# Performance work log

Measured on AMD Instinct MI355X. Metric: run time of the kernel, lower is better.

Reference implementation:

```python
import jax, jax.numpy as jnp
import numpy as np
from math import sqrt


def setup_inputs() -> dict:
    key = jax.random.key(0)
    ks = jax.random.split(key, 10)
    N, C = 192, 96  # C = N // 2
    n, h, w = 8, 64, 64
    s = lambda fan_in: 1.0 / np.sqrt(fan_in)
    return {
        "x": jax.random.normal(ks[0], (n, N, h, w), dtype=jnp.float32),
        "pe": jax.random.normal(ks[1], (N, 120, 120), dtype=jnp.float32) * 0.02,
        "wq": jax.random.normal(ks[2], (C, N), dtype=jnp.float32) * s(N),
        "bq": jax.random.normal(ks[3], (C,), dtype=jnp.float32) * 0.01,
        "wk": jax.random.normal(ks[4], (C, N), dtype=jnp.float32) * s(N),
        "bk": jax.random.normal(ks[5], (C,), dtype=jnp.float32) * 0.01,
        "wv": jax.random.normal(ks[6], (C, N), dtype=jnp.float32) * s(N),
        "bv": jax.random.normal(ks[7], (C,), dtype=jnp.float32) * 0.01,
        "wz": jax.random.normal(ks[8], (N, C), dtype=jnp.float32) * s(C),
        "bz": jax.random.normal(ks[9], (N,), dtype=jnp.float32) * 0.01,
    }


def _conv1x1(x, w, b):
    # x: [n, cin, h, w]; w: [cout, cin]; b: [cout]
    return jnp.einsum("oc,nchw->nohw", w, x) + b[None, :, None, None]


def reference(x, pe, wq, bq, wk, bk, wv, bv, wz, bz):
    n, c_in, h, w = x.shape
    hw = h * w
    # 2D positional encoding, sliced to the actual spatial size
    x = x + pe[None, :, :h, :w]
    c = wq.shape[0]  # N // 2
    q = _conv1x1(x, wq, bq).reshape(n, c, hw)   # [n, c, hw]
    k = _conv1x1(x, wk, bk).reshape(n, c, hw)   # [n, c, hw]
    v = _conv1x1(x, wv, bv).reshape(n, c, hw)   # [n, c, hw]
    scale = sqrt(hw)
    # logits[n, i, j] = sum_c q[n,c,i] * k[n,c,j]
    logits = jnp.einsum("nci,ncj->nij", q, k) / scale  # [n, hw, hw]
    weights = jax.nn.softmax(logits, axis=-1)
    # z[n, c, i] = sum_j weights[n,i,j] * v[n,c,j]
    z = jnp.einsum("nij,ncj->nci", weights, v).reshape(n, c, h, w)
    z = _conv1x1(z, wz, bz)  # [n, N, h, w]
    return x + z
```

## Files before the change

kernel.cpp:

```cpp
#include <hip/hip_runtime.h>
#include <hip/hip_bf16.h>

#define HW 4096
#define CIN 192
#define CMID 96

typedef __attribute__((ext_vector_type(8))) short bf16x8;
typedef __attribute__((ext_vector_type(4))) float f32x4;
typedef __attribute__((ext_vector_type(16))) float f32x16;
typedef __attribute__((ext_vector_type(4))) unsigned int u32x4;
typedef __attribute__((ext_vector_type(2))) unsigned int u32x2;

static __device__ __forceinline__ unsigned short f2bf(float f) {
    union { float f; unsigned int u; } v;
    v.f = f;
    unsigned int r = v.u + 0x7fffu + ((v.u >> 16) & 1u);
    return (unsigned short)(r >> 16);
}

static __device__ __forceinline__ void gload16(const void* g, void* l) {
    __builtin_amdgcn_global_load_lds(
        (const __attribute__((address_space(1))) unsigned int*)g,
        (__attribute__((address_space(3))) unsigned int*)l, 16, 0, 0);
}

#define SCQ (0.015625f * 1.44269504089f)

__global__ __launch_bounds__(256) void convw_kernel(
    const float* __restrict__ wq, const float* __restrict__ wk,
    const float* __restrict__ wv, const float* __restrict__ wz,
    unsigned short* __restrict__ wqkvb, unsigned short* __restrict__ wzb)
{
    int idx = blockIdx.x * 256 + threadIdx.x;
    if (idx < 3 * CMID * CIN) {
        int m = idx / (CMID * CIN), r = idx % (CMID * CIN);
        const float* w = (m == 0) ? wq : ((m == 1) ? wk : wv);
        wqkvb[idx] = f2bf(w[r]);
    } else if (idx < 3 * CMID * CIN + CIN * CMID) {
        int r = idx - 3 * CMID * CIN;
        wzb[r] = f2bf(wz[r]);
    }
}

__global__ __launch_bounds__(512) void qkv_kernel(
    const float* __restrict__ x, const float* __restrict__ pe,
    const unsigned short* __restrict__ wqkvb,
    const float* __restrict__ bq, const float* __restrict__ bk,
    const float* __restrict__ bv,
    unsigned short* __restrict__ Q, unsigned short* __restrict__ K,
    unsigned short* __restrict__ V)
{
    const int n = blockIdx.y, bx = blockIdx.x, i0 = bx * 64, t = threadIdx.x;
    __shared__ unsigned short xt[64 * 200];

    #pragma unroll
    for (int it = 0; it < 6; ++it) {
        int q = t + it * 512;
        int c = q >> 4, il4 = (q & 15) << 2;
        f32x4 xv = *(const f32x4*)(x + ((size_t)n * CIN + c) * HW + i0 + il4);
        f32x4 pv = *(const f32x4*)(pe + c * 14400 + bx * 120 + il4);
        float a0 = xv[0] + pv[0], a1 = xv[1] + pv[1];
        float a2 = xv[2] + pv[2], a3 = xv[3] + pv[3];
        unsigned w01, w23;
        asm("v_cvt_pk_bf16_f32 %0, %1, %2" : "=v"(w01) : "v"(a0), "v"(a1));
        asm("v_cvt_pk_bf16_f32 %0, %1, %2" : "=v"(w23) : "v"(a2), "v"(a3));
        xt[(il4 + 0) * 200 + c] = (unsigned short)w01;
        xt[(il4 + 1) * 200 + c] = (unsigned short)(w01 >> 16);
        xt[(il4 + 2) * 200 + c] = (unsigned short)w23;
        xt[(il4 + 3) * 200 + c] = (unsigned short)(w23 >> 16);
    }
    __syncthreads();

    const int w = t >> 6, lane = t & 63, l15 = lane & 15, lg = lane >> 4;
    const int wg = w >> 2;
    const int p0 = (w & 3) * 16;

    bf16x8 af[6];
    #pragma unroll
    for (int f = 0; f < 6; ++f)
        af[f] = *(const bf16x8*)(xt + (p0 + l15) * 200 + f * 32 + lg * 8);

    #pragma unroll
    for (int cc = 0; cc < 9; ++cc) {
        const int ct = wg * 9 + cc;
        const int m = ct / 6, c6 = ct % 6;
        f32x4 acc = (f32x4){0.f, 0.f, 0.f, 0.f};
        const unsigned short* wrow = wqkvb + (ct * 16 + l15) * CIN + lg * 8;
        #pragma unroll
        for (int f = 0; f < 6; ++f) {
            bf16x8 wf = *(const bf16x8*)(wrow + f * 32);
            if (m < 2)
                acc = __builtin_amdgcn_mfma_f32_16x16x32_bf16(wf, af[f], acc, 0, 0, 0);
            else
                acc = __builtin_amdgcn_mfma_f32_16x16x32_bf16(af[f], wf, acc, 0, 0, 0);
        }
        if (m < 2) {
            f32x4 bv4 = *(const f32x4*)(((m == 0) ? bq : bk) + c6 * 16 + lg * 4);
            ushort4 pk4;
            if (m == 0) {
                pk4.x = f2bf((acc[0] + bv4[0]) * SCQ);
                pk4.y = f2bf((acc[1] + bv4[1]) * SCQ);
                pk4.z = f2bf((acc[2] + bv4[2]) * SCQ);
                pk4.w = f2bf((acc[3] + bv4[3]) * SCQ);
            } else {
                pk4.x = f2bf(acc[0] + bv4[0]);
                pk4.y = f2bf(acc[1] + bv4[1]);
                pk4.z = f2bf(acc[2] + bv4[2]);
                pk4.w = f2bf(acc[3] + bv4[3]);
            }
            unsigned short* dst = ((m == 0) ? Q : K) + (size_t)n * HW * CMID;
            *(ushort4*)(dst + (size_t)(i0 + p0 + l15) * CMID + c6 * 16 + lg * 4) = pk4;
        } else {
            const float bias = bv[c6 * 16 + l15];
            ushort4 pk4;
            pk4.x = f2bf(acc[0] + bias); pk4.y = f2bf(acc[1] + bias);
            pk4.z = f2bf(acc[2] + bias); pk4.w = f2bf(acc[3] + bias);
            *(ushort4*)(V + (size_t)n * CMID * HW + (size_t)(c6 * 16 + l15) * HW
                          + i0 + p0 + lg * 4) = pk4;
        }
    }
}

__global__ __launch_bounds__(256, 2) void attn_kernel(
    const unsigned short* __restrict__ Q, const unsigned short* __restrict__ K,
    const unsigned short* __restrict__ V,
    unsigned short* __restrict__ zp, float* __restrict__ lp)
{
    const int bid = blockIdx.x;
    const int n    = bid & 7;
    const int iblk = (bid >> 3) & 15;
    const int js   = bid >> 7;

    const int t = threadIdx.x, w = t >> 6, lane = t & 63;
    const int l31 = lane & 31, hi = lane >> 5;
    const int ib = iblk * 256 + w * 64;

    __shared__ unsigned short Ks[3][32 * 128];
    __shared__ unsigned short Vs[2][96 * 64];

    const unsigned short* Qb = Q + (size_t)n * HW * CMID;
    const unsigned short* Kb = K + (size_t)n * HW * CMID;
    const unsigned short* Vb = V + (size_t)n * CMID * HW;

    bf16x8 qf[2][6];
    #pragma unroll
    for (int is = 0; is < 2; ++is)
        #pragma unroll
        for (int kc = 0; kc < 6; ++kc)
            qf[is][kc] = *(const bf16x8*)(Qb + (size_t)(ib + is * 32 + l31) * CMID
                                            + kc * 16 + hi * 8);

    int ksoff[2], vsoff[3];
    #pragma unroll
    for (int s = 0; s < 2; ++s) {
        int row = 8 * w + 4 * s + (lane >> 4);
        ksoff[s] = row * CMID + (((lane & 15) ^ (row & 7)) * 8);
    }
    #pragma unroll
    for (int s = 0; s < 3; ++s) {
        int c = 8 * (w * 3 + s) + (lane >> 3);
        vsoff[s] = c * HW + (((lane & 7) ^ (c & 7)) * 8);
    }

    const int j00 = js * 1024;

#define STAGE_K(TILE, KB) do {                                                 \
    _Pragma("unroll") for (int s = 0; s < 2; ++s)                              \
        gload16(Kb + (size_t)(j00 + (TILE) * 32) * CMID + ksoff[s],            \
                &Ks[KB][(w * 2 + s) * 512]);                                   \
} while (0)
#define STAGE_V(WND, VB) do {                                                  \
    _Pragma("unroll") for (int s = 0; s < 3; ++s)                              \
        gload16(Vb + (size_t)(j00 + (WND) * 64) + vsoff[s],                    \
                &Vs[VB][(w * 3 + s) * 512]);                                   \
} while (0)

    f32x16 O[2][3], Lon[2];
    #pragma unroll
    for (int is = 0; is < 2; ++is) {
        #pragma unroll
        for (int cc = 0; cc < 3; ++cc)
            #pragma unroll
            for (int e = 0; e < 16; ++e) O[is][cc][e] = 0.f;
        #pragma unroll
        for (int e = 0; e < 16; ++e) Lon[is][e] = 0.f;
    }

    bf16x8 onef;
    #pragma unroll
    for (int e = 0; e < 8; ++e) onef[e] = (short)0x3F80;

    STAGE_K(0, 0);
    STAGE_K(1, 1);
    STAGE_V(0, 0);
    asm volatile("s_waitcnt vmcnt(0)" ::: "memory");
    __builtin_amdgcn_s_barrier();

#define BODY(KBUF, VBUF, VHALF) do {                                           \
    const unsigned short* Kc = &Ks[KBUF][0];                                   \
    const unsigned short* Vc = &Vs[VBUF][0];                                   \
    f32x16 s0, s1;                                                             \
    _Pragma("unroll") for (int e = 0; e < 16; ++e) { s0[e] = 0.f; s1[e] = 0.f; } \
    __builtin_amdgcn_s_setprio(1);                                             \
    _Pragma("unroll") for (int kc = 0; kc < 6; ++kc) {                         \
        bf16x8 kf = *(const bf16x8*)(Kc + l31 * 128 +                          \
                      (((kc * 2 + hi) ^ (l31 & 7)) << 3));                     \
        s0 = __builtin_amdgcn_mfma_f32_32x32x16_bf16(kf, qf[0][kc], s0, 0, 0, 0); \
        s1 = __builtin_amdgcn_mfma_f32_32x32x16_bf16(kf, qf[1][kc], s1, 0, 0, 0); \
    }                                                                          \
    __builtin_amdgcn_s_setprio(0);                                             \
    unsigned pkk[2][4][2];                                                     \
    _Pragma("unroll") for (int q = 0; q < 4; ++q)                              \
        _Pragma("unroll") for (int rp = 0; rp < 2; ++rp) {                     \
            float lo0 = __builtin_exp2f(s0[q * 4 + 2 * rp]);                   \
            float hh0 = __builtin_exp2f(s0[q * 4 + 2 * rp + 1]);               \
            float lo1 = __builtin_exp2f(s1[q * 4 + 2 * rp]);                   \
            float hh1 = __builtin_exp2f(s1[q * 4 + 2 * rp + 1]);               \
            asm("v_cvt_pk_bf16_f32 %0, %1, %2"                                 \
                : "=v"(pkk[0][q][rp]) : "v"(lo0), "v"(hh0));                   \
            asm("v_cvt_pk_bf16_f32 %0, %1, %2"                                 \
                : "=v"(pkk[1][q][rp]) : "v"(lo1), "v"(hh1));                   \
        }                                                                      \
    u32x4 pfu[2][2];                                                           \
    _Pragma("unroll") for (int is = 0; is < 2; ++is)                           \
        _Pragma("unroll") for (int jc = 0; jc < 2; ++jc) {                     \
            unsigned x0 = pkk[is][2 * jc][0], y0 = pkk[is][2 * jc + 1][0];     \
            unsigned x1 = pkk[is][2 * jc][1], y1 = pkk[is][2 * jc + 1][1];     \
            asm("v_permlane32_swap_b32 %0, %1" : "+v"(y0), "+v"(x0));          \
            asm("v_permlane32_swap_b32 %0, %1" : "+v"(y1), "+v"(x1));          \
            pfu[is][jc][0] = x0; pfu[is][jc][1] = x1;                          \
            pfu[is][jc][2] = y0; pfu[is][jc][3] = y1;                          \
        }                                                                      \
    __builtin_amdgcn_s_setprio(1);                                             \
    _Pragma("unroll") for (int jc = 0; jc < 2; ++jc) {                         \
        bf16x8 pa0 = __builtin_bit_cast(bf16x8, pfu[0][jc]);                   \
        bf16x8 pa1 = __builtin_bit_cast(bf16x8, pfu[1][jc]);                   \
        _Pragma("unroll") for (int cc = 0; cc < 3; ++cc) {                     \
            bf16x8 vf = *(const bf16x8*)(Vc + (cc * 32 + l31) * 64 +           \
                          ((((VHALF) * 4 + jc * 2 + hi) ^ (l31 & 7)) << 3));   \
            O[0][cc] = __builtin_amdgcn_mfma_f32_32x32x16_bf16(pa0, vf, O[0][cc], 0, 0, 0); \
            O[1][cc] = __builtin_amdgcn_mfma_f32_32x32x16_bf16(pa1, vf, O[1][cc], 0, 0, 0); \
        }                                                                      \
        Lon[0] = __builtin_amdgcn_mfma_f32_32x32x16_bf16(pa0, onef, Lon[0], 0, 0, 0); \
        Lon[1] = __builtin_amdgcn_mfma_f32_32x32x16_bf16(pa1, onef, Lon[1], 0, 0, 0); \
    }                                                                          \
    __builtin_amdgcn_s_setprio(0);                                             \
} while (0)

    int kb = 0, kb1 = 1, kb2 = 2;
    for (int tt = 0; tt < 32; tt += 2) {
        {
            const int pfk = (tt + 2 < 32) ? tt + 2 : 31;
            STAGE_K(pfk, kb2);
            const int wn = (tt >> 1) + 1;
            const int pfw = (wn < 16) ? wn : 15;
            STAGE_V(pfw, wn & 1);
            BODY(kb, (tt >> 1) & 1, 0);
            asm volatile("s_waitcnt vmcnt(5)" ::: "memory");
            __builtin_amdgcn_s_barrier();
        }
        {
            const int pfk = (tt + 3 < 32) ? tt + 3 : 31;
            STAGE_K(pfk, kb);
            BODY(kb1, (tt >> 1) & 1, 1);
            asm volatile("s_waitcnt vmcnt(2)" ::: "memory");
            __builtin_amdgcn_s_barrier();
        }
        const int tmp = kb;
        kb = kb2; kb2 = kb1; kb1 = tmp;
    }
#undef BODY
#undef STAGE_K
#undef STAGE_V

    asm volatile("s_waitcnt vmcnt(0)" ::: "memory");

    unsigned short* zb = zp + ((size_t)js * 8 + n) * HW * CMID;
    #pragma unroll
    for (int is = 0; is < 2; ++is)
        #pragma unroll
        for (int cc = 0; cc < 3; ++cc)
            #pragma unroll
            for (int r = 0; r < 16; ++r) {
                int i = ib + is * 32 + (r & 3) + 8 * (r >> 2) + 4 * hi;
                zb[(size_t)i * CMID + cc * 32 + l31] = f2bf(O[is][cc][r]);
            }

    if (l31 == 0) {
        float* lb = lp + ((size_t)js * 8 + n) * HW;
        #pragma unroll
        for (int is = 0; is < 2; ++is)
            #pragma unroll
            for (int r = 0; r < 16; ++r) {
                int i = ib + is * 32 + (r & 3) + 8 * (r >> 2) + 4 * hi;
                lb[i] = Lon[is][r];
            }
    }
}

__global__ __launch_bounds__(256) void zproj_kernel(
    const unsigned short* __restrict__ zp, const float* __restrict__ lp,
    const unsigned short* __restrict__ wzb, const float* __restrict__ bz,
    const float* __restrict__ x, const float* __restrict__ pe,
    float* __restrict__ out)
{
    const int n = blockIdx.y, i0 = blockIdx.x * 64, t = threadIdx.x;
    __shared__ unsigned short zt[64 * 104];
    __shared__ float ll[64];

    if (t < 64) {
        float s = 0.f;
        #pragma unroll
        for (int sl = 0; sl < 4; ++sl)
            s += lp[(size_t)sl * 8 * HW + (size_t)n * HW + i0 + t];
        ll[t] = 1.f / s;
    }
    __syncthreads();

    #pragma unroll
    for (int u = 0; u < 3; ++u) {
        int unit = t + u * 256;
        int i = unit / 12, g = unit % 12;
        size_t gidx = ((size_t)n * HW + i0 + i) * CMID + g * 8;
        float a[8];
        #pragma unroll
        for (int e = 0; e < 8; ++e) a[e] = 0.f;
        #pragma unroll
        for (int sl = 0; sl < 4; ++sl) {
            u32x4 wv = *(const u32x4*)(zp + (size_t)sl * 8 * HW * CMID + gidx);
            #pragma unroll
            for (int k = 0; k < 4; ++k) {
                union { unsigned u; float f; } lo, hi2;
                lo.u = wv[k] << 16;
                hi2.u = wv[k] & 0xffff0000u;
                a[2 * k]     += lo.f;
                a[2 * k + 1] += hi2.f;
            }
        }
        float li = ll[i];
        unsigned ww[4];
        #pragma unroll
        for (int k = 0; k < 4; ++k) {
            float p0 = a[2 * k] * li, p1 = a[2 * k + 1] * li;
            asm("v_cvt_pk_bf16_f32 %0, %1, %2" : "=v"(ww[k]) : "v"(p0), "v"(p1));
        }
        u32x4 wv4 = {ww[0], ww[1], ww[2], ww[3]};
        *(u32x4*)(zt + i * 104 + g * 8) = wv4;
    }
    __syncthreads();

    const int w = t >> 6, lane = t & 63, l15 = lane & 15, lg = lane >> 4;
    const int p0 = w * 16;

    bf16x8 af[3];
    #pragma unroll
    for (int f = 0; f < 3; ++f)
        af[f] = *(const bf16x8*)(zt + (p0 + l15) * 104 + f * 32 + lg * 8);

    #pragma unroll
    for (int ct = 0; ct < 12; ++ct) {
        f32x4 acc = (f32x4){0.f, 0.f, 0.f, 0.f};
        const unsigned short* wrow = wzb + (ct * 16 + l15) * CMID + lg * 8;
        #pragma unroll
        for (int f = 0; f < 3; ++f) {
            bf16x8 wf = *(const bf16x8*)(wrow + f * 32);
            acc = __builtin_amdgcn_mfma_f32_16x16x32_bf16(af[f], wf, acc, 0, 0, 0);
        }
        const int co = ct * 16 + l15;
        const int ibase = i0 + p0 + lg * 4;
        size_t xa = ((size_t)n * CIN + co) * HW + ibase;
        f32x4 xv = *(const f32x4*)(x + xa);
        f32x4 pv = *(const f32x4*)(pe + co * 14400 + blockIdx.x * 120 + p0 + lg * 4);
        const float bias = bz[co];
        f32x4 o;
        #pragma unroll
        for (int r = 0; r < 4; ++r) o[r] = xv[r] + pv[r] + acc[r] + bias;
        *(f32x4*)(out + xa) = o;
    }
}

extern "C" void kernel_launch(void* const* d_in, const int* in_sizes, int n_in,
                              void* d_out, int out_size, void* d_ws, size_t ws_size,
                              hipStream_t stream) {
    const float* x  = (const float*)d_in[0];
    const float* pe = (const float*)d_in[1];
    const float* wq = (const float*)d_in[2];
    const float* bq = (const float*)d_in[3];
    const float* wk = (const float*)d_in[4];
    const float* bk = (const float*)d_in[5];
    const float* wv = (const float*)d_in[6];
    const float* bv = (const float*)d_in[7];
    const float* wz = (const float*)d_in[8];
    const float* bz = (const float*)d_in[9];
    float* out = (float*)d_out;

    char* ws = (char*)d_ws;
    unsigned short* wqkvb = (unsigned short*)(ws);
    unsigned short* wzb   = (unsigned short*)(ws + 131072);
    unsigned short* Qb    = (unsigned short*)(ws + 196608);
    unsigned short* Kb    = (unsigned short*)(ws + 6488064);
    unsigned short* Vb    = (unsigned short*)(ws + 12779520);
    unsigned short* zpb   = (unsigned short*)(ws + 19070976);
    float*          lpb   = (float*)(ws + 44236800);

    convw_kernel<<<288, 256, 0, stream>>>(wq, wk, wv, wz, wqkvb, wzb);
    qkv_kernel<<<dim3(64, 8), 512, 0, stream>>>(x, pe, wqkvb, bq, bk, bv,
                                                Qb, Kb, Vb);
    attn_kernel<<<512, 256, 0, stream>>>(Qb, Kb, Vb, zpb, lpb);
    zproj_kernel<<<dim3(64, 8), 256, 0, stream>>>(zpb, lpb, wzb, bz, x, pe, out);
}
```

Baseline: 126.7 us.

## Store Q/K/V in MFMA fragment layout and load directly from global

The QKV projection now writes Q, K and V in a pre-swizzled fragment-major layout, so each lane can load its MFMA operand with one contiguous 16-byte global read. The attention kernel drops the LDS staging buffers, the async global-to-LDS triple-buffer pipeline and the barriers, and reads K/V fragments straight from global/L2 each tile. The row-sum MFMA against a ones vector is replaced by scalar accumulation of the exp values plus a cross-half shuffle. This removes LDS traffic and synchronisation but loses the explicit prefetch overlap, and it relies on L2 absorbing the repeated K/V reads across the four waves.

```diff
diff --git a/kernel.cpp b/kernel.cpp
--- a/kernel.cpp
+++ b/kernel.cpp
@@ -9,19 +9,12 @@
 typedef __attribute__((ext_vector_type(4))) float f32x4;
 typedef __attribute__((ext_vector_type(16))) float f32x16;
 typedef __attribute__((ext_vector_type(4))) unsigned int u32x4;
-typedef __attribute__((ext_vector_type(2))) unsigned int u32x2;
 
 static __device__ __forceinline__ unsigned short f2bf(float f) {
     union { float f; unsigned int u; } v;
     v.f = f;
     unsigned int r = v.u + 0x7fffu + ((v.u >> 16) & 1u);
     return (unsigned short)(r >> 16);
-}
-
-static __device__ __forceinline__ void gload16(const void* g, void* l) {
-    __builtin_amdgcn_global_load_lds(
-        (const __attribute__((address_space(1))) unsigned int*)g,
-        (__attribute__((address_space(3))) unsigned int*)l, 16, 0, 0);
 }
 
 #define SCQ (0.015625f * 1.44269504089f)
@@ -47,8 +40,8 @@
     const unsigned short* __restrict__ wqkvb,
     const float* __restrict__ bq, const float* __restrict__ bk,
     const float* __restrict__ bv,
-    unsigned short* __restrict__ Q, unsigned short* __restrict__ K,
-    unsigned short* __restrict__ V)
+    unsigned short* __restrict__ QF, unsigned short* __restrict__ KF,
+    unsigned short* __restrict__ VF)
 {
     const int n = blockIdx.y, bx = blockIdx.x, i0 = bx * 64, t = threadIdx.x;
     __shared__ unsigned short xt[64 * 200];
@@ -108,22 +101,29 @@
                 pk4.z = f2bf(acc[2] + bv4[2]);
                 pk4.w = f2bf(acc[3] + bv4[3]);
             }
-            unsigned short* dst = ((m == 0) ? Q : K) + (size_t)n * HW * CMID;
-            *(ushort4*)(dst + (size_t)(i0 + p0 + l15) * CMID + c6 * 16 + lg * 4) = pk4;
+            const int p = i0 + p0 + l15;
+            unsigned short* dst = (m == 0) ? QF : KF;
+            size_t fa = ((((size_t)n * 128 + (p >> 5)) * 6 + c6) * 64
+                         + (lg >> 1) * 32 + (p & 31)) * 8 + (lg & 1) * 4;
+            *(ushort4*)(dst + fa) = pk4;
         } else {
             const float bias = bv[c6 * 16 + l15];
             ushort4 pk4;
             pk4.x = f2bf(acc[0] + bias); pk4.y = f2bf(acc[1] + bias);
             pk4.z = f2bf(acc[2] + bias); pk4.w = f2bf(acc[3] + bias);
-            *(ushort4*)(V + (size_t)n * CMID * HW + (size_t)(c6 * 16 + l15) * HW
-                          + i0 + p0 + lg * 4) = pk4;
+            const int ch = c6 * 16 + l15;
+            const int slot = 2 * (w & 3) + (lg >> 1);
+            size_t fa = ((((((size_t)n * 64 + bx) * 3 + (ch >> 5)) * 2
+                           + (slot >> 2)) * 2 + ((slot >> 1) & 1)) * 64
+                         + (slot & 1) * 32 + (ch & 31)) * 8 + (lg & 1) * 4;
+            *(ushort4*)(VF + fa) = pk4;
         }
     }
 }
 
 __global__ __launch_bounds__(256, 2) void attn_kernel(
-    const unsigned short* __restrict__ Q, const unsigned short* __restrict__ K,
-    const unsigned short* __restrict__ V,
+    const unsigned short* __restrict__ QF, const unsigned short* __restrict__ KF,
+    const unsigned short* __restrict__ VF,
     unsigned short* __restrict__ zp, float* __restrict__ lp)
 {
     const int bid = blockIdx.x;
@@ -135,145 +135,98 @@
     const int l31 = lane & 31, hi = lane >> 5;
     const int ib = iblk * 256 + w * 64;
 
-    __shared__ unsigned short Ks[3][32 * 128];
-    __shared__ unsigned short Vs[2][96 * 64];
-
-    const unsigned short* Qb = Q + (size_t)n * HW * CMID;
-    const unsigned short* Kb = K + (size_t)n * HW * CMID;
-    const unsigned short* Vb = V + (size_t)n * CMID * HW;
+    const unsigned short* QFb = QF + (size_t)n * 128 * 3072;
+    const unsigned short* KFb = KF + (size_t)n * 128 * 3072;
+    const unsigned short* VFb = VF + (size_t)n * 64 * 6144;
 
     bf16x8 qf[2][6];
     #pragma unroll
     for (int is = 0; is < 2; ++is)
         #pragma unroll
         for (int kc = 0; kc < 6; ++kc)
-            qf[is][kc] = *(const bf16x8*)(Qb + (size_t)(ib + is * 32 + l31) * CMID
-                                            + kc * 16 + hi * 8);
-
-    int ksoff[2], vsoff[3];
-    #pragma unroll
-    for (int s = 0; s < 2; ++s) {
-        int row = 8 * w + 4 * s + (lane >> 4);
-        ksoff[s] = row * CMID + (((lane & 15) ^ (row & 7)) * 8);
-    }
-    #pragma unroll
-    for (int s = 0; s < 3; ++s) {
-        int c = 8 * (w * 3 + s) + (lane >> 3);
-        vsoff[s] = c * HW + (((lane & 7) ^ (c & 7)) * 8);
-    }
-
-    const int j00 = js * 1024;
-
-#define STAGE_K(TILE, KB) do {                                                 \
-    _Pragma("unroll") for (int s = 0; s < 2; ++s)                              \
-        gload16(Kb + (size_t)(j00 + (TILE) * 32) * CMID + ksoff[s],            \
-                &Ks[KB][(w * 2 + s) * 512]);                                   \
-} while (0)
-#define STAGE_V(WND, VB) do {                                                  \
-    _Pragma("unroll") for (int s = 0; s < 3; ++s)                              \
-        gload16(Vb + (size_t)(j00 + (WND) * 64) + vsoff[s],                    \
-                &Vs[VB][(w * 3 + s) * 512]);                                   \
-} while (0)
-
-    f32x16 O[2][3], Lon[2];
-    #pragma unroll
-    for (int is = 0; is < 2; ++is) {
+            qf[is][kc] = *(const bf16x8*)(QFb + ((size_t)((ib >> 5) + is) * 6 + kc) * 512
+                                          + lane * 8);
+
+    f32x16 O[2][3];
+    #pragma unroll
+    for (int is = 0; is < 2; ++is)
         #pragma unroll
         for (int cc = 0; cc < 3; ++cc)
             #pragma unroll
             for (int e = 0; e < 16; ++e) O[is][cc][e] = 0.f;
-        #pragma unroll
-        for (int e = 0; e < 16; ++e) Lon[is][e] = 0.f;
-    }
-
-    bf16x8 onef;
-    #pragma unroll
-    for (int e = 0; e < 8; ++e) onef[e] = (short)0x3F80;
-
-    STAGE_K(0, 0);
-    STAGE_K(1, 1);
-    STAGE_V(0, 0);
-    asm volatile("s_waitcnt vmcnt(0)" ::: "memory");
-    __builtin_amdgcn_s_barrier();
-
-#define BODY(KBUF, VBUF, VHALF) do {                                           \
-    const unsigned short* Kc = &Ks[KBUF][0];                                   \
-    const unsigned short* Vc = &Vs[VBUF][0];                                   \
-    f32x16 s0, s1;                                                             \
-    _Pragma("unroll") for (int e = 0; e < 16; ++e) { s0[e] = 0.f; s1[e] = 0.f; } \
-    __builtin_amdgcn_s_setprio(1);                                             \
-    _Pragma("unroll") for (int kc = 0; kc < 6; ++kc) {                         \
-        bf16x8 kf = *(const bf16x8*)(Kc + l31 * 128 +                          \
-                      (((kc * 2 + hi) ^ (l31 & 7)) << 3));                     \
-        s0 = __builtin_amdgcn_mfma_f32_32x32x16_bf16(kf, qf[0][kc], s0, 0, 0, 0); \
-        s1 = __builtin_amdgcn_mfma_f32_32x32x16_bf16(kf, qf[1][kc], s1, 0, 0, 0); \
-    }                                                                          \
-    __builtin_amdgcn_s_setprio(0);                                             \
-    unsigned pkk[2][4][2];                                                     \
-    _Pragma("unroll") for (int q = 0; q < 4; ++q)                              \
-        _Pragma("unroll") for (int rp = 0; rp < 2; ++rp) {                     \
-            float lo0 = __builtin_exp2f(s0[q * 4 + 2 * rp]);                   \
-            float hh0 = __builtin_exp2f(s0[q * 4 + 2 * rp + 1]);               \
-            float lo1 = __builtin_exp2f(s1[q * 4 + 2 * rp]);                   \
-            float hh1 = __builtin_exp2f(s1[q * 4 + 2 * rp + 1]);               \
-            asm("v_cvt_pk_bf16_f32 %0, %1, %2"                                 \
-                : "=v"(pkk[0][q][rp]) : "v"(lo0), "v"(hh0));                   \
-            asm("v_cvt_pk_bf16_f32 %0, %1, %2"                                 \
-                : "=v"(pkk[1][q][rp]) : "v"(lo1), "v"(hh1));                   \
-        }                                                                      \
-    u32x4 pfu[2][2];                                                           \
-    _Pragma("unroll") for (int is = 0; is < 2; ++is)                           \
-        _Pragma("unroll") for (int jc = 0; jc < 2; ++jc) {                     \
-            unsigned x0 = pkk[is][2 * jc][0], y0 = pkk[is][2 * jc + 1][0];     \
-            unsigned x1 = pkk[is][2 * jc][1], y1 = pkk[is][2 * jc + 1][1];     \
-            asm("v_permlane32_swap_b32 %0, %1" : "+v"(y0), "+v"(x0));          \
-            asm("v_permlane32_swap_b32 %0, %1" : "+v"(y1), "+v"(x1));          \
-            pfu[is][jc][0] = x0; pfu[is][jc][1] = x1;                          \
-            pfu[is][jc][2] = y0; pfu[is][jc][3] = y1;                          \
-        }                                                                      \
-    __builtin_amdgcn_s_setprio(1);                                             \
-    _Pragma("unroll") for (int jc = 0; jc < 2; ++jc) {                         \
-        bf16x8 pa0 = __builtin_bit_cast(bf16x8, pfu[0][jc]);                   \
-        bf16x8 pa1 = __builtin_bit_cast(bf16x8, pfu[1][jc]);                   \
-        _Pragma("unroll") for (int cc = 0; cc < 3; ++cc) {                     \
-            bf16x8 vf = *(const bf16x8*)(Vc + (cc * 32 + l31) * 64 +           \
-                          ((((VHALF) * 4 + jc * 2 + hi) ^ (l31 & 7)) << 3));   \
-            O[0][cc] = __builtin_amdgcn_mfma_f32_32x32x16_bf16(pa0, vf, O[0][cc], 0, 0, 0); \
-            O[1][cc] = __builtin_amdgcn_mfma_f32_32x32x16_bf16(pa1, vf, O[1][cc], 0, 0, 0); \
-        }                                                                      \
-        Lon[0] = __builtin_amdgcn_mfma_f32_32x32x16_bf16(pa0, onef, Lon[0], 0, 0, 0); \
-        Lon[1] = __builtin_amdgcn_mfma_f32_32x32x16_bf16(pa1, onef, Lon[1], 0, 0, 0); \
-    }                                                                          \
-    __builtin_amdgcn_s_setprio(0);                                             \
-} while (0)
-
-    int kb = 0, kb1 = 1, kb2 = 2;
-    for (int tt = 0; tt < 32; tt += 2) {
-        {
-            const int pfk = (tt + 2 < 32) ? tt + 2 : 31;
-            STAGE_K(pfk, kb2);
-            const int wn = (tt >> 1) + 1;
-            const int pfw = (wn < 16) ? wn : 15;
-            STAGE_V(pfw, wn & 1);
-            BODY(kb, (tt >> 1) & 1, 0);
-            asm volatile("s_waitcnt vmcnt(5)" ::: "memory");
-            __builtin_amdgcn_s_barrier();
-        }
-        {
-            const int pfk = (tt + 3 < 32) ? tt + 3 : 31;
-            STAGE_K(pfk, kb);
-            BODY(kb1, (tt >> 1) & 1, 1);
-            asm volatile("s_waitcnt vmcnt(2)" ::: "memory");
-            __builtin_amdgcn_s_barrier();
-        }
-        const int tmp = kb;
-        kb = kb2; kb2 = kb1; kb1 = tmp;
-    }
-#undef BODY
-#undef STAGE_K
-#undef STAGE_V
-
-    asm volatile("s_waitcnt vmcnt(0)" ::: "memory");
+    float lsum0 = 0.f, lsum1 = 0.f;
+
+    for (int tt = 0; tt < 32; ++tt) {
+        const int jt = js * 32 + tt;
+        const unsigned short* Kt = KFb + (size_t)jt * 3072;
+
+        bf16x8 kf[6];
+        #pragma unroll
+        for (int kc = 0; kc < 6; ++kc)
+            kf[kc] = *(const bf16x8*)(Kt + kc * 512 + lane * 8);
+        bf16x8 vf[2][3];
+        #pragma unroll
+        for (int jc = 0; jc < 2; ++jc)
+            #pragma unroll
+            for (int cc = 0; cc < 3; ++cc)
+                vf[jc][cc] = *(const bf16x8*)(VFb
+                    + ((size_t)((jt >> 1) * 3 + cc) * 4 + (jt & 1) * 2 + jc) * 512
+                    + lane * 8);
+
+        f32x16 s0, s1;
+        #pragma unroll
+        for (int e = 0; e < 16; ++e) { s0[e] = 0.f; s1[e] = 0.f; }
+        __builtin_amdgcn_s_setprio(1);
+        #pragma unroll
+        for (int kc = 0; kc < 6; ++kc) {
+            s0 = __builtin_amdgcn_mfma_f32_32x32x16_bf16(kf[kc], qf[0][kc], s0, 0, 0, 0);
+            s1 = __builtin_amdgcn_mfma_f32_32x32x16_bf16(kf[kc], qf[1][kc], s1, 0, 0, 0);
+        }
+        __builtin_amdgcn_s_setprio(0);
+
+        unsigned pkk[2][4][2];
+        #pragma unroll
+        for (int q = 0; q < 4; ++q)
+            #pragma unroll
+            for (int rp = 0; rp < 2; ++rp) {
+                float lo0 = __builtin_exp2f(s0[q * 4 + 2 * rp]);
+                float hh0 = __builtin_exp2f(s0[q * 4 + 2 * rp + 1]);
+                float lo1 = __builtin_exp2f(s1[q * 4 + 2 * rp]);
+                float hh1 = __builtin_exp2f(s1[q * 4 + 2 * rp + 1]);
+                lsum0 += lo0 + hh0;
+                lsum1 += lo1 + hh1;
+                asm("v_cvt_pk_bf16_f32 %0, %1, %2"
+                    : "=v"(pkk[0][q][rp]) : "v"(lo0), "v"(hh0));
+                asm("v_cvt_pk_bf16_f32 %0, %1, %2"
+                    : "=v"(pkk[1][q][rp]) : "v"(lo1), "v"(hh1));
+            }
+
+        u32x4 pfu[2][2];
+        #pragma unroll
+        for (int is = 0; is < 2; ++is)
+            #pragma unroll
+            for (int jc = 0; jc < 2; ++jc) {
+                unsigned x0 = pkk[is][2 * jc][0], y0 = pkk[is][2 * jc + 1][0];
+                unsigned x1 = pkk[is][2 * jc][1], y1 = pkk[is][2 * jc + 1][1];
+                asm("v_permlane32_swap_b32 %0, %1" : "+v"(y0), "+v"(x0));
+                asm("v_permlane32_swap_b32 %0, %1" : "+v"(y1), "+v"(x1));
+                pfu[is][jc][0] = x0; pfu[is][jc][1] = x1;
+                pfu[is][jc][2] = y0; pfu[is][jc][3] = y1;
+            }
+
+        __builtin_amdgcn_s_setprio(1);
+        #pragma unroll
+        for (int jc = 0; jc < 2; ++jc) {
+            bf16x8 pa0 = __builtin_bit_cast(bf16x8, pfu[0][jc]);
+            bf16x8 pa1 = __builtin_bit_cast(bf16x8, pfu[1][jc]);
+            #pragma unroll
+            for (int cc = 0; cc < 3; ++cc) {
+                O[0][cc] = __builtin_amdgcn_mfma_f32_32x32x16_bf16(pa0, vf[jc][cc], O[0][cc], 0, 0, 0);
+                O[1][cc] = __builtin_amdgcn_mfma_f32_32x32x16_bf16(pa1, vf[jc][cc], O[1][cc], 0, 0, 0);
+            }
+        }
+        __builtin_amdgcn_s_setprio(0);
+    }
 
     unsigned short* zb = zp + ((size_t)js * 8 + n) * HW * CMID;
     #pragma unroll
@@ -286,15 +239,12 @@
                 zb[(size_t)i * CMID + cc * 32 + l31] = f2bf(O[is][cc][r]);
             }
 
-    if (l31 == 0) {
+    lsum0 += __shfl_xor(lsum0, 32, 64);
+    lsum1 += __shfl_xor(lsum1, 32, 64);
+    if (hi == 0) {
         float* lb = lp + ((size_t)js * 8 + n) * HW;
-        #pragma unroll
-        for (int is = 0; is < 2; ++is)
-            #pragma unroll
-            for (int r = 0; r < 16; ++r) {
-                int i = ib + is * 32 + (r & 3) + 8 * (r >> 2) + 4 * hi;
-                lb[i] = Lon[is][r];
-            }
+        lb[ib + l31]      = lsum0;
+        lb[ib + 32 + l31] = lsum1;
     }
 }
 
@@ -397,15 +347,15 @@
     char* ws = (char*)d_ws;
     unsigned short* wqkvb = (unsigned short*)(ws);
     unsigned short* wzb   = (unsigned short*)(ws + 131072);
-    unsigned short* Qb    = (unsigned short*)(ws + 196608);
-    unsigned short* Kb    = (unsigned short*)(ws + 6488064);
-    unsigned short* Vb    = (unsigned short*)(ws + 12779520);
+    unsigned short* QFb   = (unsigned short*)(ws + 196608);
+    unsigned short* KFb   = (unsigned short*)(ws + 6488064);
+    unsigned short* VFb   = (unsigned short*)(ws + 12779520);
     unsigned short* zpb   = (unsigned short*)(ws + 19070976);
     float*          lpb   = (float*)(ws + 44236800);
 
     convw_kernel<<<288, 256, 0, stream>>>(wq, wk, wv, wz, wqkvb, wzb);
     qkv_kernel<<<dim3(64, 8), 512, 0, stream>>>(x, pe, wqkvb, bq, bk, bv,
-                                                Qb, Kb, Vb);
-    attn_kernel<<<512, 256, 0, stream>>>(Qb, Kb, Vb, zpb, lpb);
+                                                QFb, KFb, VFb);
+    attn_kernel<<<512, 256, 0, stream>>>(QFb, KFb, VFb, zpb, lpb);
     zproj_kernel<<<dim3(64, 8), 256, 0, stream>>>(zpb, lpb, wzb, bz, x, pe, out);
 }
```

New measurement: 118.0 us, median of 2. -6.9%, faster.
